# Performance work log

Hardware: AMD Instinct MI355X
Metric: run time of the kernel (lower is better)

The kernel has to match this reference:

```python
import jax, jax.numpy as jnp
import numpy as np

DM = 1024        # model dim
NEXPERTS = 32    # experts per set; also group size t for the token permutation
EXPERTSETS = 4
EXPERTSIZE = 32  # dff = NEXPERTS * EXPERTSETS * EXPERTSIZE = 4096
BATCH, SEQ = 4, 2048


def setup_inputs() -> dict:
    key = jax.random.key(0)
    k0, k1, k2, k3 = jax.random.split(key, 4)
    scale = 0.02
    x = jax.random.normal(k0, (BATCH, SEQ, DM), jnp.float32)
    controller = jax.random.normal(k1, (DM, NEXPERTS, EXPERTSETS), jnp.float32) * scale
    f1 = jax.random.normal(k2, (DM, NEXPERTS, EXPERTSETS, EXPERTSIZE), jnp.float32) * scale
    bias = jnp.zeros((NEXPERTS, EXPERTSETS, EXPERTSIZE), jnp.float32)
    f2 = jax.random.normal(k3, (NEXPERTS, EXPERTSETS, EXPERTSIZE, DM), jnp.float32) * scale
    return {"x": x, "controller": controller, "f1": f1, "bias": bias, "f2": f2}


def reference(x, controller, f1, bias, f2):
    B, L, d = x.shape
    t = controller.shape[1]            # nexperts == group size
    g = L // t                         # number of token groups per example
    grouped = x.reshape(B, g, t, d)    # '... (b t) d -> ... b t d'

    # controller logits: '... t d, d e s -> ... t e s'
    logits = jnp.einsum('bgtd,des->bgtes', grouped, controller)
    # deterministic tiebreak over the token axis t (dim -3)
    tie = jnp.linspace(0.0, 1e-6, t, dtype=logits.dtype).reshape(t, 1, 1)
    logits = logits + tie
    # one-hot-ish permutation: for each (e, s) slot pick the argmax token in the group
    perm = (logits == jnp.max(logits, axis=-3, keepdims=True)).astype(x.dtype)
    perm = jax.lax.stop_gradient(perm)  # torch eq() produces detached bool mask

    # einsum 1 ('... t d, d e s f, ... t e s -> ... e s f'), done in the efficient order:
    # dispatch tokens to expert slots first, then the per-expert GEMM
    dispatched = jnp.einsum('bgtd,bgtes->bgesd', grouped, perm)
    inner = jax.nn.relu(jnp.einsum('bgesd,desf->bgesf', dispatched, f1) + bias)

    # einsum 2 + unpermute
    intermediate = jnp.einsum('bgesf,esfd->bgesd', inner, f2)
    out = jnp.einsum('bgesd,bgtes->bgtd', intermediate, perm)

    return out.reshape(B, L, d)
```

## Files before the change

### kernel.cpp

```cpp
#include <hip/hip_runtime.h>
#include <hip/hip_bf16.h>

#define NGROUP 256
#define NSLOT  128
#define TG     32
#define DM     1024
#define FF     32

#define LSCALE     4096.0f
#define INV_LSCALE (1.0f / 4096.0f)

typedef unsigned int  uint;
typedef unsigned short ushort;
typedef unsigned char uchar;
typedef __attribute__((ext_vector_type(4))) float f32x4;
typedef __attribute__((ext_vector_type(8))) short bf16x8;
typedef __attribute__((ext_vector_type(8))) _Float16 f16x8;

__device__ __forceinline__ ushort f2bf(float f) {
    uint u = __float_as_uint(f);
    u += 0x7FFFu + ((u >> 16) & 1u);
    return (ushort)(u >> 16);
}
__device__ __forceinline__ uint pk2(float a, float b) {
    return (uint)f2bf(a) | ((uint)f2bf(b) << 16);
}

__device__ __forceinline__ void gload_lds16(const void* g, void* l) {
    __builtin_amdgcn_global_load_lds(
        (const __attribute__((address_space(1))) uint*)g,
        (__attribute__((address_space(3))) uint*)l, 16, 0, 0);
}

__global__ __launch_bounds__(256) void k_fused1(
    const float* __restrict__ x, const float* __restrict__ ctrl,
    const float* __restrict__ f1, const float* __restrict__ f2,
    int* __restrict__ idx, uchar* __restrict__ idx8, ushort* __restrict__ xb,
    ushort* __restrict__ f1F, ushort* __restrict__ f2T)
{
    __shared__ float smem[4 * 32 * 64];
    const int t = threadIdx.x;

    if (blockIdx.x < 512) {
        float* Lp = smem;
        const int g  = blockIdx.x >> 1;
        const int nh = blockIdx.x & 1;
        const int w = t >> 6;
        const int lane = t & 63;
        const int lrow = lane & 15;
        const int lk8 = (lane >> 4) * 8;

        const size_t xoff0 = ((size_t)g * TG + lrow) * DM + w * 256 + lk8;
        const float* xr0 = x + xoff0;
        const float* xr1 = xr0 + 16 * DM;

        f32x4 ahh[2][4], ax[2][4];
#pragma unroll
        for (int mt = 0; mt < 2; ++mt)
#pragma unroll
            for (int nt = 0; nt < 4; ++nt) {
                ahh[mt][nt] = (f32x4){0.f, 0.f, 0.f, 0.f};
                ax[mt][nt]  = (f32x4){0.f, 0.f, 0.f, 0.f};
            }

        for (int ks = 0; ks < 8; ++ks) {
            f16x8 Ah[2], Al[2];
#pragma unroll
            for (int mt = 0; mt < 2; ++mt) {
                const float* p = (mt ? xr1 : xr0) + ks * 32;
                float xe[8];
                *(float4*)&xe[0] = *(const float4*)p;
                *(float4*)&xe[4] = *(const float4*)(p + 4);
                union { f16x8 v; _Float16 e[8]; } H, L;
#pragma unroll
                for (int j = 0; j < 8; ++j) {
                    const _Float16 h = (_Float16)xe[j];
                    H.e[j] = h;
                    L.e[j] = (_Float16)((xe[j] - (float)h) * LSCALE);
                }
                Ah[mt] = H.v; Al[mt] = L.v;
                if (nh == 0) {
                    uint4 o;
                    o.x = pk2(xe[0], xe[1]); o.y = pk2(xe[2], xe[3]);
                    o.z = pk2(xe[4], xe[5]); o.w = pk2(xe[6], xe[7]);
                    *(uint4*)(xb + xoff0 + (size_t)mt * 16 * DM + ks * 32) = o;
                }
            }
            const int kslice = w * 8 + ks;
#pragma unroll
            for (int nt = 0; nt < 4; ++nt) {
                const float* cp = ctrl
                    + (size_t)(kslice * 32 + ((lane >> 4) << 3)) * NSLOT
                    + nh * 64 + nt * 16 + (lane & 15);
                union { f16x8 v; _Float16 e[8]; } BH, BL;
#pragma unroll
                for (int j = 0; j < 8; ++j) {
                    const float c = cp[(size_t)j * NSLOT];
                    const _Float16 h = (_Float16)c;
                    BH.e[j] = h;
                    BL.e[j] = (_Float16)((c - (float)h) * LSCALE);
                }
#pragma unroll
                for (int mt = 0; mt < 2; ++mt) {
                    ahh[mt][nt] = __builtin_amdgcn_mfma_f32_16x16x32_f16(Ah[mt], BH.v, ahh[mt][nt], 0, 0, 0);
                    ax[mt][nt]  = __builtin_amdgcn_mfma_f32_16x16x32_f16(Al[mt], BH.v, ax[mt][nt], 0, 0, 0);
                    ax[mt][nt]  = __builtin_amdgcn_mfma_f32_16x16x32_f16(Ah[mt], BL.v, ax[mt][nt], 0, 0, 0);
                }
            }
        }

#pragma unroll
        for (int mt = 0; mt < 2; ++mt)
#pragma unroll
            for (int nt = 0; nt < 4; ++nt)
#pragma unroll
                for (int r = 0; r < 4; ++r) {
                    const int trow = mt * 16 + (lane >> 4) * 4 + r;
                    const int nl = nt * 16 + lrow;
                    Lp[(w * TG + trow) * 64 + nl] =
                        ahh[mt][nt][r] + ax[mt][nt][r] * INV_LSCALE;
                }
        __syncthreads();

        for (int i = t * 4; i < TG * 64; i += 256 * 4) {
            f32x4 s0 = *(const f32x4*)&Lp[i];
            f32x4 s1 = *(const f32x4*)&Lp[2048 + i];
            f32x4 s2 = *(const f32x4*)&Lp[4096 + i];
            f32x4 s3 = *(const f32x4*)&Lp[6144 + i];
            *(f32x4*)&Lp[i] = (s0 + s1) + (s2 + s3);
        }
        __syncthreads();

        if (t < 64) {
            const int n = t;
            float best = -1e30f;
            int bi = 0;
#pragma unroll
            for (int tt = 0; tt < TG; ++tt) {
                const float v = Lp[tt * 64 + n] + (float)tt * (1e-6f / 31.0f);
                if (v >= best) { best = v; bi = tt; }
            }
            idx[g * NSLOT + nh * 64 + n] = bi;
            idx8[g * NSLOT + nh * 64 + n] = (uchar)bi;
        }
    } else if (blockIdx.x < 768) {
        float* Ltr = smem;
        const int i1 = blockIdx.x - 512;
        const int es = i1 >> 1;
        const int dh = i1 & 1;
        for (int d0 = dh * 512; d0 < dh * 512 + 512; d0 += 64) {
            const int dd = t >> 2, f0 = (t & 3) * 8;
            const float* src = f1 + (size_t)(d0 + dd) * 4096 + es * FF + f0;
            float4 a = *(const float4*)src;
            float4 b = *(const float4*)(src + 4);
            __syncthreads();
            float* Lq = &Ltr[dd * 33 + f0];
            Lq[0] = a.x; Lq[1] = a.y; Lq[2] = a.z; Lq[3] = a.w;
            Lq[4] = b.x; Lq[5] = b.y; Lq[6] = b.z; Lq[7] = b.w;
            __syncthreads();
            const int f = t & 31, koct = t >> 5;
            const int nt = f >> 4;
            const int kg = d0 + koct * 8;
            const int kslice = kg >> 5;
            const int lane2 = (f & 15) | (((kg >> 3) & 3) << 4);
            uint4 o;
            o.x = pk2(Ltr[(koct * 8 + 0) * 33 + f], Ltr[(koct * 8 + 1) * 33 + f]);
            o.y = pk2(Ltr[(koct * 8 + 2) * 33 + f], Ltr[(koct * 8 + 3) * 33 + f]);
            o.z = pk2(Ltr[(koct * 8 + 4) * 33 + f], Ltr[(koct * 8 + 5) * 33 + f]);
            o.w = pk2(Ltr[(koct * 8 + 6) * 33 + f], Ltr[(koct * 8 + 7) * 33 + f]);
            *(uint4*)(f1F + ((((size_t)es * 2 + nt) * 32 + kslice) * 64 + lane2) * 8) = o;
        }
    } else {
        float* Ltr = smem;
        const int i2 = blockIdx.x - 768;
        const int es = i2 >> 2;
        const int dq = i2 & 3;
        for (int d0 = dq * 256; d0 < dq * 256 + 256; d0 += 64) {
            const int f = t >> 3, ds = (t & 7) * 8;
            const float* src = f2 + (size_t)es * (FF * DM) + f * DM + d0 + ds;
            float4 a = *(const float4*)src;
            float4 b = *(const float4*)(src + 4);
            __syncthreads();
            Ltr[(ds + 0) * 33 + f] = a.x; Ltr[(ds + 1) * 33 + f] = a.y;
            Ltr[(ds + 2) * 33 + f] = a.z; Ltr[(ds + 3) * 33 + f] = a.w;
            Ltr[(ds + 4) * 33 + f] = b.x; Ltr[(ds + 5) * 33 + f] = b.y;
            Ltr[(ds + 6) * 33 + f] = b.z; Ltr[(ds + 7) * 33 + f] = b.w;
            __syncthreads();
            const int dd = t >> 2, f0 = (t & 3) * 8;
            uint4 o;
            o.x = pk2(Ltr[dd * 33 + f0 + 0], Ltr[dd * 33 + f0 + 1]);
            o.y = pk2(Ltr[dd * 33 + f0 + 2], Ltr[dd * 33 + f0 + 3]);
            o.z = pk2(Ltr[dd * 33 + f0 + 4], Ltr[dd * 33 + f0 + 5]);
            o.w = pk2(Ltr[dd * 33 + f0 + 6], Ltr[dd * 33 + f0 + 7]);
            *(uint4*)(f2T + (size_t)es * (FF * DM) + (d0 + dd) * FF + f0) = o;
        }
    }
}

__global__ __launch_bounds__(256) void k_h_mfma(
    const ushort* __restrict__ xb, const ushort* __restrict__ f1F,
    const float* __restrict__ bias, const int* __restrict__ idx,
    ushort* __restrict__ HbT)
{
    const int es = blockIdx.x >> 2;
    const int gq = blockIdx.x & 3;
    const int w = threadIdx.x >> 6;
    const int lane = threadIdx.x & 63;
    const int lrow = lane & 15;
    const int lk8 = (lane >> 4) * 8;

    const int ga = gq * 64 + w * 16 + lrow;
    const int tok = idx[ga * NSLOT + es];
    const ushort* abase = xb + ((size_t)ga * TG + tok) * DM + lk8;
    const ushort* bbase = f1F + (size_t)es * 2 * 32 * 512 + (size_t)lane * 8;

    f32x4 acc[2] = {(f32x4){0.f, 0.f, 0.f, 0.f}, (f32x4){0.f, 0.f, 0.f, 0.f}};

#pragma unroll 4
    for (int kslice = 0; kslice < 32; ++kslice) {
        const bf16x8 A = *(const bf16x8*)(abase + kslice * 32);
#pragma unroll
        for (int nt = 0; nt < 2; ++nt) {
            const bf16x8 B = *(const bf16x8*)(bbase + ((size_t)nt * 32 + kslice) * 512);
            acc[nt] = __builtin_amdgcn_mfma_f32_16x16x32_bf16(A, B, acc[nt], 0, 0, 0);
        }
    }

#pragma unroll
    for (int nt = 0; nt < 2; ++nt) {
        const int f = nt * 16 + lrow;
        const float bv = bias[es * FF + f];
#pragma unroll
        for (int r = 0; r < 4; ++r) {
            const int g = gq * 64 + w * 16 + (lane >> 4) * 4 + r;
            const float hv = fmaxf(acc[nt][r] + bv, 0.0f);
            HbT[(size_t)es * (NGROUP * FF) + g * FF + f] = f2bf(hv);
        }
    }
}

__global__ __launch_bounds__(256) void k_out_mfma(
    const ushort* __restrict__ HbT, const ushort* __restrict__ f2T,
    const uchar* __restrict__ idx8, float* __restrict__ out)
{
    extern __shared__ char smK3[];
    float* OL   = (float*)smK3;
    char*  Ring = smK3 + 131072;

    const int D0 = (blockIdx.x & 15) * 64;
    const int G0 = (blockIdx.x >> 4) * 16;
    const int tid = threadIdx.x;
    const int w = tid >> 6;
    const int lane = tid & 63;
    const int gl = lane & 15;
    const int sq = lane >> 4;
    const int dq = w * 4 + sq;

    for (int i = tid * 4; i < 32768; i += 1024)
        *(f32x4*)&OL[i] = (f32x4){0.f, 0.f, 0.f, 0.f};
    uint ui[32];
    {
        const uint4* p = (const uint4*)(idx8 + (size_t)(G0 + gl) * NSLOT);
#pragma unroll
        for (int k = 0; k < 8; ++k) {
            const uint4 v = p[k];
            ui[k * 4 + 0] = v.x; ui[k * 4 + 1] = v.y;
            ui[k * 4 + 2] = v.z; ui[k * 4 + 3] = v.w;
        }
    }
    __syncthreads();

    const ushort* ap  = f2T + (size_t)(D0 + w * 16 + gl) * FF + sq * 8;
    const ushort* bps = HbT + (size_t)(G0 + gl) * FF + sq * 8;
    char* ring = Ring + w * 8192;

#pragma unroll
    for (int s = 0; s < 3; ++s) {
        gload_lds16(ap  + (size_t)s * (FF * DM),     ring + s * 2048);
        gload_lds16(bps + (size_t)s * (NGROUP * FF), ring + s * 2048 + 1024);
    }

    const int sOL = (dq << 4) | (dq ^ gl);

#pragma unroll 4
    for (int e = 0; e < 128; ++e) {
        {
            const int en = (e + 3) & 127;
            char* slot = ring + ((e + 3) & 3) * 2048;
            gload_lds16(ap  + (size_t)en * (FF * DM),     slot);
            gload_lds16(bps + (size_t)en * (NGROUP * FF), slot + 1024);
        }
        asm volatile("s_waitcnt vmcnt(6)" ::: "memory");

        const char* slot = ring + (e & 3) * 2048;
        const bf16x8 afr = *(const bf16x8*)(slot + lane * 16);
        const bf16x8 bfr = *(const bf16x8*)(slot + 1024 + lane * 16);
        const f32x4 d = __builtin_amdgcn_mfma_f32_16x16x32_bf16(
            afr, bfr, (f32x4){0.f, 0.f, 0.f, 0.f}, 0, 0, 0);
        const uint tv = (ui[e >> 2] >> ((e & 3) * 8)) & 0xFFu;
        float* olp = &OL[tv * 1024 + sOL * 4];
        *(f32x4*)olp = *(const f32x4*)olp + d;
    }
    asm volatile("s_waitcnt vmcnt(0)" ::: "memory");
    __syncthreads();

    {
        const int g = tid >> 4, dqe = tid & 15;
        const int se = (dqe << 4) | (dqe ^ g);
#pragma unroll 4
        for (int t = 0; t < TG; ++t) {
            const f32x4 v = *(const f32x4*)&OL[t * 1024 + se * 4];
            *(f32x4*)&out[((size_t)(G0 + g) * TG + t) * DM + D0 + dqe * 4] = v;
        }
    }
}

extern "C" void kernel_launch(void* const* d_in, const int* in_sizes, int n_in,
                              void* d_out, int out_size, void* d_ws, size_t ws_size,
                              hipStream_t stream) {
    (void)in_sizes; (void)n_in; (void)out_size; (void)ws_size;
    const float* x    = (const float*)d_in[0];
    const float* ctrl = (const float*)d_in[1];
    const float* f1   = (const float*)d_in[2];
    const float* bias = (const float*)d_in[3];
    const float* f2   = (const float*)d_in[4];
    float* out = (float*)d_out;

    char* ws = (char*)d_ws;
    int*    idx  = (int*)ws;
    ushort* HbT  = (ushort*)(ws + 131072);
    ushort* f1F  = (ushort*)(ws + 2228224);
    ushort* f2T  = (ushort*)(ws + 10616832);
    ushort* xb   = (ushort*)(ws + 19005440);
    uchar*  idx8 = (uchar*)(ws + 35782656);

    k_fused1<<<1280, 256, 0, stream>>>(x, ctrl, f1, f2, idx, idx8, xb, f1F, f2T);

    k_h_mfma<<<NSLOT * 4, 256, 0, stream>>>(xb, f1F, bias, idx, HbT);

    const size_t lds3 = 163840;
    hipFuncSetAttribute((const void*)k_out_mfma,
                        hipFuncAttributeMaxDynamicSharedMemorySize, (int)lds3);
    k_out_mfma<<<256, 256, lds3, stream>>>(HbT, f2T, idx8, out);
}
```

Before: 68.76 us.

## Move f2 transpose into second kernel and batch controller loads

```diff
diff --git a/kernel.cpp b/kernel.cpp
--- a/kernel.cpp
+++ b/kernel.cpp
@@ -34,9 +34,9 @@
 
 __global__ __launch_bounds__(256) void k_fused1(
     const float* __restrict__ x, const float* __restrict__ ctrl,
-    const float* __restrict__ f1, const float* __restrict__ f2,
+    const float* __restrict__ f1,
     int* __restrict__ idx, uchar* __restrict__ idx8, ushort* __restrict__ xb,
-    ushort* __restrict__ f1F, ushort* __restrict__ f2T)
+    ushort* __restrict__ f1F)
 {
     __shared__ float smem[4 * 32 * 64];
     const int t = threadIdx.x;
@@ -87,15 +87,22 @@
                 }
             }
             const int kslice = w * 8 + ks;
+            float craw[4][8];
 #pragma unroll
             for (int nt = 0; nt < 4; ++nt) {
                 const float* cp = ctrl
                     + (size_t)(kslice * 32 + ((lane >> 4) << 3)) * NSLOT
                     + nh * 64 + nt * 16 + (lane & 15);
+#pragma unroll
+                for (int j = 0; j < 8; ++j)
+                    craw[nt][j] = cp[(size_t)j * NSLOT];
+            }
+#pragma unroll
+            for (int nt = 0; nt < 4; ++nt) {
                 union { f16x8 v; _Float16 e[8]; } BH, BL;
 #pragma unroll
                 for (int j = 0; j < 8; ++j) {
-                    const float c = cp[(size_t)j * NSLOT];
+                    const float c = craw[nt][j];
                     const _Float16 h = (_Float16)c;
                     BH.e[j] = h;
                     BL.e[j] = (_Float16)((c - (float)h) * LSCALE);
@@ -143,7 +150,7 @@
             idx[g * NSLOT + nh * 64 + n] = bi;
             idx8[g * NSLOT + nh * 64 + n] = (uchar)bi;
         }
-    } else if (blockIdx.x < 768) {
+    } else {
         float* Ltr = smem;
         const int i1 = blockIdx.x - 512;
         const int es = i1 >> 1;
@@ -170,9 +177,56 @@
             o.w = pk2(Ltr[(koct * 8 + 6) * 33 + f], Ltr[(koct * 8 + 7) * 33 + f]);
             *(uint4*)(f1F + ((((size_t)es * 2 + nt) * 32 + kslice) * 64 + lane2) * 8) = o;
         }
+    }
+}
+
+__global__ __launch_bounds__(256) void k_h_mfma(
+    const ushort* __restrict__ xb, const ushort* __restrict__ f1F,
+    const float* __restrict__ bias, const int* __restrict__ idx,
+    const float* __restrict__ f2,
+    ushort* __restrict__ HbT, ushort* __restrict__ f2T)
+{
+    __shared__ float Ltr[64 * 33];
+    const int t = threadIdx.x;
+
+    if (blockIdx.x < 512) {
+        const int es = blockIdx.x >> 2;
+        const int gq = blockIdx.x & 3;
+        const int w = t >> 6;
+        const int lane = t & 63;
+        const int lrow = lane & 15;
+        const int lk8 = (lane >> 4) * 8;
+
+        const int ga = gq * 64 + w * 16 + lrow;
+        const int tok = idx[ga * NSLOT + es];
+        const ushort* abase = xb + ((size_t)ga * TG + tok) * DM + lk8;
+        const ushort* bbase = f1F + (size_t)es * 2 * 32 * 512 + (size_t)lane * 8;
+
+        f32x4 acc[2] = {(f32x4){0.f, 0.f, 0.f, 0.f}, (f32x4){0.f, 0.f, 0.f, 0.f}};
+
+#pragma unroll 4
+        for (int kslice = 0; kslice < 32; ++kslice) {
+            const bf16x8 A = *(const bf16x8*)(abase + kslice * 32);
+#pragma unroll
+            for (int nt = 0; nt < 2; ++nt) {
+                const bf16x8 B = *(const bf16x8*)(bbase + ((size_t)nt * 32 + kslice) * 512);
+                acc[nt] = __builtin_amdgcn_mfma_f32_16x16x32_bf16(A, B, acc[nt], 0, 0, 0);
+            }
+        }
+
+#pragma unroll
+        for (int nt = 0; nt < 2; ++nt) {
+            const int f = nt * 16 + lrow;
+            const float bv = bias[es * FF + f];
+#pragma unroll
+            for (int r = 0; r < 4; ++r) {
+                const int g = gq * 64 + w * 16 + (lane >> 4) * 4 + r;
+                const float hv = fmaxf(acc[nt][r] + bv, 0.0f);
+                HbT[(size_t)es * (NGROUP * FF) + g * FF + f] = f2bf(hv);
+            }
+        }
     } else {
-        float* Ltr = smem;
-        const int i2 = blockIdx.x - 768;
+        const int i2 = blockIdx.x - 512;
         const int es = i2 >> 2;
         const int dq = i2 & 3;
         for (int d0 = dq * 256; d0 < dq * 256 + 256; d0 += 64) {
@@ -197,48 +251,6 @@
     }
 }
 
-__global__ __launch_bounds__(256) void k_h_mfma(
-    const ushort* __restrict__ xb, const ushort* __restrict__ f1F,
-    const float* __restrict__ bias, const int* __restrict__ idx,
-    ushort* __restrict__ HbT)
-{
-    const int es = blockIdx.x >> 2;
-    const int gq = blockIdx.x & 3;
-    const int w = threadIdx.x >> 6;
-    const int lane = threadIdx.x & 63;
-    const int lrow = lane & 15;
-    const int lk8 = (lane >> 4) * 8;
-
-    const int ga = gq * 64 + w * 16 + lrow;
-    const int tok = idx[ga * NSLOT + es];
-    const ushort* abase = xb + ((size_t)ga * TG + tok) * DM + lk8;
-    const ushort* bbase = f1F + (size_t)es * 2 * 32 * 512 + (size_t)lane * 8;
-
-    f32x4 acc[2] = {(f32x4){0.f, 0.f, 0.f, 0.f}, (f32x4){0.f, 0.f, 0.f, 0.f}};
-
-#pragma unroll 4
-    for (int kslice = 0; kslice < 32; ++kslice) {
-        const bf16x8 A = *(const bf16x8*)(abase + kslice * 32);
-#pragma unroll
-        for (int nt = 0; nt < 2; ++nt) {
-            const bf16x8 B = *(const bf16x8*)(bbase + ((size_t)nt * 32 + kslice) * 512);
-            acc[nt] = __builtin_amdgcn_mfma_f32_16x16x32_bf16(A, B, acc[nt], 0, 0, 0);
-        }
-    }
-
-#pragma unroll
-    for (int nt = 0; nt < 2; ++nt) {
-        const int f = nt * 16 + lrow;
-        const float bv = bias[es * FF + f];
-#pragma unroll
-        for (int r = 0; r < 4; ++r) {
-            const int g = gq * 64 + w * 16 + (lane >> 4) * 4 + r;
-            const float hv = fmaxf(acc[nt][r] + bv, 0.0f);
-            HbT[(size_t)es * (NGROUP * FF) + g * FF + f] = f2bf(hv);
-        }
-    }
-}
-
 __global__ __launch_bounds__(256) void k_out_mfma(
     const ushort* __restrict__ HbT, const ushort* __restrict__ f2T,
     const uchar* __restrict__ idx8, float* __restrict__ out)
@@ -334,9 +346,9 @@
     ushort* xb   = (ushort*)(ws + 19005440);
     uchar*  idx8 = (uchar*)(ws + 35782656);
 
-    k_fused1<<<1280, 256, 0, stream>>>(x, ctrl, f1, f2, idx, idx8, xb, f1F, f2T);
-
-    k_h_mfma<<<NSLOT * 4, 256, 0, stream>>>(xb, f1F, bias, idx, HbT);
+    k_fused1<<<768, 256, 0, stream>>>(x, ctrl, f1, idx, idx8, xb, f1F);
+
+    k_h_mfma<<<1024, 256, 0, stream>>>(xb, f1F, bias, idx, f2, HbT, f2T);
 
     const size_t lds3 = 163840;
     hipFuncSetAttribute((const void*)k_out_mfma,
```

New measurement: 68.37 us. No clear change (-0.6%).
